# Optimization experiments

Hardware: AMD Instinct MI355X
Metric: run time of the kernel (lower is better)

Reference implementation:

```python
import jax, jax.numpy as jnp
import numpy as np

B = 524288   # number of samples scored at inference
K = 8        # GMM mixture components
D = 16       # latent feature dim (AE code + reconstruction-error features)


def setup_inputs() -> dict:
    key = jax.random.key(0)
    k1, k2, k3, k4 = jax.random.split(key, 4)
    z = jax.random.normal(k1, (B, D), dtype=jnp.float32)
    mu = jax.random.normal(k2, (K, D), dtype=jnp.float32)
    # sigma must be SPD (it is an estimated covariance + 0.001*I in the original);
    # build it as A A^T / D + 0.1*I so cholesky succeeds and densities are sane.
    A = jax.random.normal(k3, (K, D, D), dtype=jnp.float32) / np.sqrt(D)
    sigma = jnp.einsum('kij,klj->kil', A, A) + 0.1 * jnp.eye(D, dtype=jnp.float32)
    logits = jax.random.normal(k4, (K,), dtype=jnp.float32)
    mixture_probabilities = jax.nn.softmax(logits)
    return {"mu": mu, "sigma": sigma, "z": z,
            "mixture_probabilities": mixture_probabilities}


def reference(mu, sigma, z, mixture_probabilities):
    # Faithful to compute_sample_energy: per-sample MVN density for each of K
    # components via Cholesky, weighted by mixture probs, summed, -log.
    # Vectorized: one batched triangular solve instead of tf.map_fn per sample.
    d = z.shape[-1]
    L = jnp.linalg.cholesky(sigma)                      # [K,D,D]
    diff = z[:, None, :] - mu[None, :, :]               # [B,K,D]
    diff_t = jnp.transpose(diff, (1, 2, 0))             # [K,D,B]
    y = jax.scipy.linalg.solve_triangular(L, diff_t, lower=True)  # [K,D,B]
    maha = jnp.sum(y * y, axis=1)                       # [K,B] Mahalanobis dist
    log_det = jnp.sum(jnp.log(jnp.diagonal(L, axis1=-2, axis2=-1)), axis=-1)  # [K]
    log_norm = -0.5 * d * jnp.log(jnp.asarray(2.0 * np.pi, dtype=z.dtype))
    log_prob = log_norm - log_det[:, None] - 0.5 * maha  # [K,B]
    densities = jnp.exp(log_prob).T                      # [B,K] == map_fn(prob)
    energy = -jnp.log(jnp.sum(densities * mixture_probabilities, axis=1))  # [B]
    return energy
```

## Files before the change

### kernel.cpp

```cpp
#include <hip/hip_runtime.h>
#include <math.h>

#define KCOMP 8
#define DDIM  16

typedef __attribute__((ext_vector_type(8))) short bf16x8;
typedef __attribute__((ext_vector_type(4))) float f32x4;

static __device__ __forceinline__ unsigned short f2bf(float f) {
    unsigned u = __float_as_uint(f);
    unsigned r = (u + 0x7FFFu + ((u >> 16) & 1u)) >> 16;
    return (unsigned short)r;
}

__global__ __launch_bounds__(128) void prep_kernel(
    const float* __restrict__ mu, const float* __restrict__ sigma,
    const float* __restrict__ pi, float* __restrict__ ws)
{
    __shared__ float sLinv[KCOMP * DDIM * DDIM];
    __shared__ float sB[KCOMP * DDIM];
    __shared__ float sC[KCOMP];

    const int tid = threadIdx.x;
    const int g = tid >> 4;
    const int r = tid & 15;

    float a[DDIM];
    const float4* srow = (const float4*)(sigma + g * DDIM * DDIM + r * DDIM);
    float4 v0 = srow[0], v1 = srow[1], v2 = srow[2], v3 = srow[3];
    a[0]=v0.x;  a[1]=v0.y;  a[2]=v0.z;  a[3]=v0.w;
    a[4]=v1.x;  a[5]=v1.y;  a[6]=v1.z;  a[7]=v1.w;
    a[8]=v2.x;  a[9]=v2.y;  a[10]=v2.z; a[11]=v2.w;
    a[12]=v3.x; a[13]=v3.y; a[14]=v3.z; a[15]=v3.w;

    float l[DDIM];
    #pragma unroll
    for (int j = 0; j < DDIM; ++j) {
        float s = a[j];
        #pragma unroll
        for (int m2 = 0; m2 < j; ++m2)
            s -= l[m2] * __shfl(l[m2], j, DDIM);
        float dj = sqrtf(__shfl(s, j, DDIM));
        float val;
        if (r == j)      val = dj;
        else if (r > j)  val = s / dj;
        else             val = 0.0f;
        l[j] = val;
    }

    float x[DDIM];
    #pragma unroll
    for (int i = 0; i < DDIM; ++i) {
        float t = (r == i) ? 1.0f : 0.0f;
        #pragma unroll
        for (int m2 = 0; m2 < i; ++m2)
            t -= __shfl(l[m2], i, DDIM) * x[m2];
        x[i] = t / __shfl(l[i], i, DDIM);
    }

    #pragma unroll
    for (int i = 0; i < DDIM; ++i)
        sLinv[g * 256 + i * DDIM + r] = x[i];

    float b = 0.0f;
    #pragma unroll
    for (int c = 0; c < DDIM; ++c)
        b += sLinv[g * 256 + r * DDIM + c] * mu[g * DDIM + c];
    sB[g * DDIM + r] = b;

    float ld = logf(l[r]);
    #pragma unroll
    for (int off = 8; off >= 1; off >>= 1)
        ld += __shfl_xor(ld, off, DDIM);
    if (r == 0) {
        const float LOG2PI = 1.8378770664093454f;
        sC[g] = logf(pi[g]) - ld - 0.5f * DDIM * LOG2PI;
    }
    __syncthreads();

    #pragma unroll
    for (int i = 0; i < 4; ++i) {
        const int e    = tid + i * 128;
        const int k    = e >> 6;
        const int lane = e & 63;
        const int m    = lane & 15;
        const int quad = lane >> 4;
        float vals[8];
        #pragma unroll
        for (int j = 0; j < 8; ++j) vals[j] = 0.0f;
        if (quad < 2) {
            #pragma unroll
            for (int j = 0; j < 8; ++j)
                vals[j] = sLinv[k * 256 + m * DDIM + quad * 8 + j];
        } else if (quad == 2) {
            vals[0] = -sB[k * DDIM + m];
        }
        uint4 p;
        p.x = (unsigned)f2bf(vals[0]) | ((unsigned)f2bf(vals[1]) << 16);
        p.y = (unsigned)f2bf(vals[2]) | ((unsigned)f2bf(vals[3]) << 16);
        p.z = (unsigned)f2bf(vals[4]) | ((unsigned)f2bf(vals[5]) << 16);
        p.w = (unsigned)f2bf(vals[6]) | ((unsigned)f2bf(vals[7]) << 16);
        ((uint4*)ws)[e] = p;
    }
    if (tid < KCOMP) ws[2048 + tid] = sC[tid];
}

__global__ __launch_bounds__(256, 4) void energy_kernel(
    const float* __restrict__ z, const float* __restrict__ ws,
    float* __restrict__ out, int n)
{
    const int tid  = threadIdx.x;
    const int lane = tid & 63;
    const int m    = lane & 15;
    const int quad = lane >> 4;
    const int base = ((blockIdx.x * 256 + tid) >> 6) * 64;

    bf16x8 afrag[KCOMP];
    #pragma unroll
    for (int k = 0; k < KCOMP; ++k)
        afrag[k] = ((const bf16x8*)ws)[k * 64 + lane];

    float ck[KCOMP];
    #pragma unroll
    for (int k = 0; k < KCOMP; ++k) ck[k] = ws[2048 + k];

    bf16x8 bfrag[4];
    #pragma unroll
    for (int t = 0; t < 4; ++t) {
        bf16x8 bf = {0,0,0,0,0,0,0,0};
        const int s = base + t * 16 + m;
        if (quad < 2) {
            if (s < n) {
                const float4* zp = (const float4*)(z + (size_t)s * DDIM + quad * 8);
                float4 w0 = zp[0], w1 = zp[1];
                bf[0]=(short)f2bf(w0.x); bf[1]=(short)f2bf(w0.y);
                bf[2]=(short)f2bf(w0.z); bf[3]=(short)f2bf(w0.w);
                bf[4]=(short)f2bf(w1.x); bf[5]=(short)f2bf(w1.y);
                bf[6]=(short)f2bf(w1.z); bf[7]=(short)f2bf(w1.w);
            }
        } else if (quad == 2) {
            bf[0] = (short)0x3F80;
        }
        bfrag[t] = bf;
    }

    const f32x4 zero4 = {0.f, 0.f, 0.f, 0.f};
    float lp[KCOMP];

    #pragma unroll
    for (int t = 0; t < 4; ++t) {
        #pragma unroll
        for (int k = 0; k < KCOMP; ++k) {
            f32x4 d4 = __builtin_amdgcn_mfma_f32_16x16x32_bf16(
                           afrag[k], bfrag[t], zero4, 0, 0, 0);
            float p = d4[0]*d4[0] + d4[1]*d4[1] + d4[2]*d4[2] + d4[3]*d4[3];
            p += __shfl_xor(p, 16, 64);
            p += __shfl_xor(p, 32, 64);
            float lpv = fmaf(-0.5f, p, ck[k]);
            if (t == 0) lp[k] = lpv;
            else        lp[k] = (quad == t) ? lpv : lp[k];
        }
    }

    float mx = lp[0];
    #pragma unroll
    for (int k = 1; k < KCOMP; ++k) mx = fmaxf(mx, lp[k]);
    float dens = 0.0f;
    #pragma unroll
    for (int k = 0; k < KCOMP; ++k) dens += __expf(lp[k] - mx);

    const int so = base + lane;
    if (so < n) out[so] = -(mx + __logf(dens));
}

extern "C" void kernel_launch(void* const* d_in, const int* in_sizes, int n_in,
                              void* d_out, int out_size, void* d_ws, size_t ws_size,
                              hipStream_t stream) {
    const float* mu    = (const float*)d_in[0];
    const float* sigma = (const float*)d_in[1];
    const float* z     = (const float*)d_in[2];
    const float* pi    = (const float*)d_in[3];
    float* ws  = (float*)d_ws;
    float* out = (float*)d_out;

    const int n = in_sizes[2] / DDIM;

    prep_kernel<<<1, 128, 0, stream>>>(mu, sigma, pi, ws);

    const int blocks = (n + 255) / 256;
    energy_kernel<<<blocks, 256, 0, stream>>>(z, ws, out, n);
}
```

Measured before the change: 94.44 us.

## Fuse Cholesky prep into energy kernel and truncate z to bf16

Merges the single-block Cholesky/inverse prep kernel into the main energy kernel, so every block recomputes the per-component factors into shared memory. This removes one launch and the dependency through the workspace buffer. The cost is redundant per-block work: 2048 blocks each run the serial 16x16 Cholesky and triangular inverse on two warps before a barrier. It also replaces round-to-nearest bf16 conversion of z with plain truncation, which is cheaper but slightly less accurate.

After: 102.6 us. 8.6% more time.

```diff
diff --git a/kernel.cpp b/kernel.cpp
--- a/kernel.cpp
+++ b/kernel.cpp
@@ -7,109 +7,93 @@
 typedef __attribute__((ext_vector_type(8))) short bf16x8;
 typedef __attribute__((ext_vector_type(4))) float f32x4;
 
-static __device__ __forceinline__ unsigned short f2bf(float f) {
+static __device__ __forceinline__ unsigned short f2bf_rne(float f) {
     unsigned u = __float_as_uint(f);
     unsigned r = (u + 0x7FFFu + ((u >> 16) & 1u)) >> 16;
     return (unsigned short)r;
 }
 
-__global__ __launch_bounds__(128) void prep_kernel(
+__global__ __launch_bounds__(256, 4) void dagmm_kernel(
     const float* __restrict__ mu, const float* __restrict__ sigma,
-    const float* __restrict__ pi, float* __restrict__ ws)
+    const float* __restrict__ pi, const float* __restrict__ z,
+    float* __restrict__ out, int n)
 {
-    __shared__ float sLinv[KCOMP * DDIM * DDIM];
-    __shared__ float sB[KCOMP * DDIM];
+    __shared__ uint4 sAfrag[KCOMP * 64];
     __shared__ float sC[KCOMP];
 
     const int tid = threadIdx.x;
-    const int g = tid >> 4;
-    const int r = tid & 15;
 
-    float a[DDIM];
-    const float4* srow = (const float4*)(sigma + g * DDIM * DDIM + r * DDIM);
-    float4 v0 = srow[0], v1 = srow[1], v2 = srow[2], v3 = srow[3];
-    a[0]=v0.x;  a[1]=v0.y;  a[2]=v0.z;  a[3]=v0.w;
-    a[4]=v1.x;  a[5]=v1.y;  a[6]=v1.z;  a[7]=v1.w;
-    a[8]=v2.x;  a[9]=v2.y;  a[10]=v2.z; a[11]=v2.w;
-    a[12]=v3.x; a[13]=v3.y; a[14]=v3.z; a[15]=v3.w;
+    if (tid < 128) {
+        const int g = tid >> 4;
+        const int r = tid & 15;
 
-    float l[DDIM];
-    #pragma unroll
-    for (int j = 0; j < DDIM; ++j) {
-        float s = a[j];
+        float a[DDIM];
+        const float4* srow = (const float4*)(sigma + g * DDIM * DDIM + r * DDIM);
+        float4 v0 = srow[0], v1 = srow[1], v2 = srow[2], v3 = srow[3];
+        a[0]=v0.x;  a[1]=v0.y;  a[2]=v0.z;  a[3]=v0.w;
+        a[4]=v1.x;  a[5]=v1.y;  a[6]=v1.z;  a[7]=v1.w;
+        a[8]=v2.x;  a[9]=v2.y;  a[10]=v2.z; a[11]=v2.w;
+        a[12]=v3.x; a[13]=v3.y; a[14]=v3.z; a[15]=v3.w;
+
+        float l[DDIM];
         #pragma unroll
-        for (int m2 = 0; m2 < j; ++m2)
-            s -= l[m2] * __shfl(l[m2], j, DDIM);
-        float dj = sqrtf(__shfl(s, j, DDIM));
-        float val;
-        if (r == j)      val = dj;
-        else if (r > j)  val = s / dj;
-        else             val = 0.0f;
-        l[j] = val;
-    }
+        for (int j = 0; j < DDIM; ++j) {
+            float s = a[j];
+            #pragma unroll
+            for (int m2 = 0; m2 < j; ++m2)
+                s -= l[m2] * __shfl(l[m2], j, DDIM);
+            float dj = sqrtf(__shfl(s, j, DDIM));
+            float val;
+            if (r == j)      val = dj;
+            else if (r > j)  val = s / dj;
+            else             val = 0.0f;
+            l[j] = val;
+        }
 
-    float x[DDIM];
-    #pragma unroll
-    for (int i = 0; i < DDIM; ++i) {
-        float t = (r == i) ? 1.0f : 0.0f;
+        float x[DDIM];
         #pragma unroll
-        for (int m2 = 0; m2 < i; ++m2)
-            t -= __shfl(l[m2], i, DDIM) * x[m2];
-        x[i] = t / __shfl(l[i], i, DDIM);
-    }
+        for (int i = 0; i < DDIM; ++i) {
+            float t = (r == i) ? 1.0f : 0.0f;
+            #pragma unroll
+            for (int m2 = 0; m2 < i; ++m2)
+                t -= __shfl(l[m2], i, DDIM) * x[m2];
+            x[i] = t / __shfl(l[i], i, DDIM);
+        }
 
-    #pragma unroll
-    for (int i = 0; i < DDIM; ++i)
-        sLinv[g * 256 + i * DDIM + r] = x[i];
+        float b = 0.0f;
+        #pragma unroll
+        for (int c = 0; c < DDIM; ++c)
+            b += __shfl(x[r], c, DDIM) * mu[g * DDIM + c];
 
-    float b = 0.0f;
-    #pragma unroll
-    for (int c = 0; c < DDIM; ++c)
-        b += sLinv[g * 256 + r * DDIM + c] * mu[g * DDIM + c];
-    sB[g * DDIM + r] = b;
+        float ld = logf(l[r]);
+        #pragma unroll
+        for (int off = 8; off >= 1; off >>= 1)
+            ld += __shfl_xor(ld, off, DDIM);
+        if (r == 0) {
+            const float LOG2PI = 1.8378770664093454f;
+            sC[g] = logf(pi[g]) - ld - 0.5f * DDIM * LOG2PI;
+        }
 
-    float ld = logf(l[r]);
-    #pragma unroll
-    for (int off = 8; off >= 1; off >>= 1)
-        ld += __shfl_xor(ld, off, DDIM);
-    if (r == 0) {
-        const float LOG2PI = 1.8378770664093454f;
-        sC[g] = logf(pi[g]) - ld - 0.5f * DDIM * LOG2PI;
+        #pragma unroll
+        for (int quad = 0; quad < 4; ++quad) {
+            float vals[8];
+            #pragma unroll
+            for (int j = 0; j < 8; ++j) {
+                int c = quad * 8 + j;
+                float lv = (quad < 2) ? __shfl(x[r], c, DDIM) : 0.0f;
+                if (quad == 2 && j == 0) lv = -b;
+                vals[j] = lv;
+            }
+            uint4 p;
+            p.x = (unsigned)f2bf_rne(vals[0]) | ((unsigned)f2bf_rne(vals[1]) << 16);
+            p.y = (unsigned)f2bf_rne(vals[2]) | ((unsigned)f2bf_rne(vals[3]) << 16);
+            p.z = (unsigned)f2bf_rne(vals[4]) | ((unsigned)f2bf_rne(vals[5]) << 16);
+            p.w = (unsigned)f2bf_rne(vals[6]) | ((unsigned)f2bf_rne(vals[7]) << 16);
+            sAfrag[g * 64 + quad * 16 + r] = p;
+        }
     }
     __syncthreads();
 
-    #pragma unroll
-    for (int i = 0; i < 4; ++i) {
-        const int e    = tid + i * 128;
-        const int k    = e >> 6;
-        const int lane = e & 63;
-        const int m    = lane & 15;
-        const int quad = lane >> 4;
-        float vals[8];
-        #pragma unroll
-        for (int j = 0; j < 8; ++j) vals[j] = 0.0f;
-        if (quad < 2) {
-            #pragma unroll
-            for (int j = 0; j < 8; ++j)
-                vals[j] = sLinv[k * 256 + m * DDIM + quad * 8 + j];
-        } else if (quad == 2) {
-            vals[0] = -sB[k * DDIM + m];
-        }
-        uint4 p;
-        p.x = (unsigned)f2bf(vals[0]) | ((unsigned)f2bf(vals[1]) << 16);
-        p.y = (unsigned)f2bf(vals[2]) | ((unsigned)f2bf(vals[3]) << 16);
-        p.z = (unsigned)f2bf(vals[4]) | ((unsigned)f2bf(vals[5]) << 16);
-        p.w = (unsigned)f2bf(vals[6]) | ((unsigned)f2bf(vals[7]) << 16);
-        ((uint4*)ws)[e] = p;
-    }
-    if (tid < KCOMP) ws[2048 + tid] = sC[tid];
-}
-
-__global__ __launch_bounds__(256, 4) void energy_kernel(
-    const float* __restrict__ z, const float* __restrict__ ws,
-    float* __restrict__ out, int n)
-{
-    const int tid  = threadIdx.x;
     const int lane = tid & 63;
     const int m    = lane & 15;
     const int quad = lane >> 4;
@@ -118,11 +102,11 @@
     bf16x8 afrag[KCOMP];
     #pragma unroll
     for (int k = 0; k < KCOMP; ++k)
-        afrag[k] = ((const bf16x8*)ws)[k * 64 + lane];
+        afrag[k] = ((const bf16x8*)sAfrag)[k * 64 + lane];
 
     float ck[KCOMP];
     #pragma unroll
-    for (int k = 0; k < KCOMP; ++k) ck[k] = ws[2048 + k];
+    for (int k = 0; k < KCOMP; ++k) ck[k] = sC[k];
 
     bf16x8 bfrag[4];
     #pragma unroll
@@ -133,10 +117,14 @@
             if (s < n) {
                 const float4* zp = (const float4*)(z + (size_t)s * DDIM + quad * 8);
                 float4 w0 = zp[0], w1 = zp[1];
-                bf[0]=(short)f2bf(w0.x); bf[1]=(short)f2bf(w0.y);
-                bf[2]=(short)f2bf(w0.z); bf[3]=(short)f2bf(w0.w);
-                bf[4]=(short)f2bf(w1.x); bf[5]=(short)f2bf(w1.y);
-                bf[6]=(short)f2bf(w1.z); bf[7]=(short)f2bf(w1.w);
+                bf[0]=(short)(__float_as_uint(w0.x) >> 16);
+                bf[1]=(short)(__float_as_uint(w0.y) >> 16);
+                bf[2]=(short)(__float_as_uint(w0.z) >> 16);
+                bf[3]=(short)(__float_as_uint(w0.w) >> 16);
+                bf[4]=(short)(__float_as_uint(w1.x) >> 16);
+                bf[5]=(short)(__float_as_uint(w1.y) >> 16);
+                bf[6]=(short)(__float_as_uint(w1.z) >> 16);
+                bf[7]=(short)(__float_as_uint(w1.w) >> 16);
             }
         } else if (quad == 2) {
             bf[0] = (short)0x3F80;
@@ -180,13 +168,11 @@
     const float* sigma = (const float*)d_in[1];
     const float* z     = (const float*)d_in[2];
     const float* pi    = (const float*)d_in[3];
-    float* ws  = (float*)d_ws;
     float* out = (float*)d_out;
+    (void)d_ws; (void)ws_size;
 
     const int n = in_sizes[2] / DDIM;
 
-    prep_kernel<<<1, 128, 0, stream>>>(mu, sigma, pi, ws);
-
     const int blocks = (n + 255) / 256;
-    energy_kernel<<<blocks, 256, 0, stream>>>(z, ws, out, n);
+    dagmm_kernel<<<blocks, 256, 0, stream>>>(mu, sigma, pi, z, out, n);
 }
```
